# Performance work log

Measured on AMD Instinct MI355X. Metric: run time of the kernel, lower is better.

The kernel has to match this reference:

```python
import jax, jax.numpy as jnp
import numpy as np

B, T, N, E, H, L, K = 2, 32, 256, 1024, 16, 2, 256
MAXLEN = 512  # RelativeMultiheadAttention max_seq_len default
SCALES = (1, 2, 4)
TAU = 1.0


def setup_inputs() -> dict:
    key = jax.random.key(0)
    ks = jax.random.split(key, 9)
    s = 0.02
    A = 2 * L  # [layer0-spatial, layer0-temporal, layer1-spatial, layer1-temporal]
    return {
        "x": jax.random.normal(ks[0], (B, T, N, E), jnp.float32),
        "attn_wq": jax.random.normal(ks[1], (A, E, E), jnp.float32) * s,
        "attn_bq": jnp.zeros((A, E), jnp.float32),
        "attn_wk": jax.random.normal(ks[2], (A, E, E), jnp.float32) * s,
        "attn_bk": jnp.zeros((A, E), jnp.float32),
        "attn_wv": jax.random.normal(ks[3], (A, E, E), jnp.float32) * s,
        "attn_bv": jnp.zeros((A, E), jnp.float32),
        "attn_wd": jax.random.normal(ks[4], (A, E, E), jnp.float32) * s,
        "attn_bd": jnp.zeros((A, E), jnp.float32),
        "rel_bias": jax.random.normal(ks[5], (A, 2 * MAXLEN - 1, H), jnp.float32) * s,
        "sel_w": jax.random.normal(ks[6], (E, K), jnp.float32) * s,
        "sel_b": jnp.zeros((K,), jnp.float32),
    }


def _rel_attn(x, wq, bq, wk, bk, wv, bv, wd, bd, rb):
    # x: [Bx, S, E]; rb: [2*MAXLEN-1, H]
    Bx, S, _ = x.shape
    D = E // H
    q = (x @ wq + bq).reshape(Bx, S, H, D)
    k = (x @ wk + bk).reshape(Bx, S, H, D)
    v = (x @ wv + bv).reshape(Bx, S, H, D)
    scores = jnp.einsum('bshd,bthd->bhst', q, k) / jnp.sqrt(jnp.asarray(D, x.dtype))
    pos = jnp.arange(S)
    idx = pos[None, :] - pos[:, None] + (MAXLEN - 1)  # [S, S]
    bias = rb[idx]  # [S, S, H] gathered relative-position bias
    scores = scores + bias.transpose(2, 0, 1)[None]
    w = jax.nn.softmax(scores, axis=-1)
    ctx = jnp.einsum('bhst,bthd->bshd', w, v).reshape(Bx, S, E)
    return ctx @ wd + bd


def reference(x, attn_wq, attn_bq, attn_wk, attn_bk, attn_wv, attn_bv,
              attn_wd, attn_bd, rel_bias, sel_w, sel_b):
    h = x
    for l in range(L):
        # spatial attention over tokens within each frame
        i = 2 * l
        hs = h.reshape(B * T, N, E)
        hs = _rel_attn(hs, attn_wq[i], attn_bq[i], attn_wk[i], attn_bk[i],
                       attn_wv[i], attn_bv[i], attn_wd[i], attn_bd[i], rel_bias[i])
        # temporal attention across frames per spatial location
        j = 2 * l + 1
        ht = hs.reshape(B, T, N, E).transpose(0, 2, 1, 3).reshape(B * N, T, E)
        ht = _rel_attn(ht, attn_wq[j], attn_bq[j], attn_wk[j], attn_bk[j],
                       attn_wv[j], attn_bv[j], attn_wd[j], attn_bd[j], rel_bias[j])
        h = ht.reshape(B, N, T, E).transpose(0, 2, 1, 3)
    # DifferentiableTokenSelection: softmax-weighted pooling into K tokens
    flat = h.reshape(B, T * N, E)
    sc = flat @ sel_w + sel_b  # [B, T*N, K]
    wts = jax.nn.softmax(sc / TAU, axis=1)
    sel = jnp.einsum('bmk,bme->bke', wts, flat)  # [B, K, E]
    # multi-scale average pooling (kernel==stride==scale), concat along tokens
    outs = [sel.reshape(B, K // s, s, E).mean(axis=2) for s in SCALES]
    return jnp.concatenate(outs, axis=1)  # [B, K + K//2 + K//4, E]
```

## Files before the change

### kernel.cpp

```cpp
#include <hip/hip_runtime.h>
#include <stdint.h>


using f16x8 = __attribute__((ext_vector_type(8))) _Float16;
using f16x4 = __attribute__((ext_vector_type(4))) _Float16;
using f32x4 = __attribute__((ext_vector_type(4))) float;

__device__ __forceinline__ int tmap_dev(int m) {
    int bx = m >> 5;
    int s  = m & 31;
    int b  = bx >> 8;
    int n  = bx & 255;
    return (((b << 5) + s) << 8) + n;
}

__device__ __forceinline__ void load16(const _Float16* g, _Float16* l)
{
    __builtin_amdgcn_global_load_lds(
        (const __attribute__((address_space(1))) unsigned int*)g,
        (__attribute__((address_space(3))) unsigned int*)l,
        16, 0, 0);
}

__device__ __forceinline__ void split_f16(float v, _Float16& h, _Float16& l)
{
    h = (_Float16)v;
    l = (_Float16)(v - (float)h);
}

__global__ __launch_bounds__(256)
void conv_act(const float* __restrict__ src, _Float16* __restrict__ dh,
              _Float16* __restrict__ dl, int m_off)
{
    int idx = blockIdx.x * 256 + threadIdx.x;
    int e = idx << 3;
    int ml = e >> 10, col = e & 1023;
    const float* s = src + (size_t)(m_off + ml) * 1024 + col;
    float4 a = *(const float4*)s;
    float4 b = *(const float4*)(s + 4);
    float vv[8] = {a.x, a.y, a.z, a.w, b.x, b.y, b.z, b.w};
    f16x8 vh, vl;
    #pragma unroll
    for (int r = 0; r < 8; r++) {
        _Float16 h, l;
        split_f16(vv[r], h, l);
        vh[r] = h; vl[r] = l;
    }
    *(f16x8*)(dh + (size_t)ml * 1024 + col) = vh;
    *(f16x8*)(dl + (size_t)ml * 1024 + col) = vl;
}

__global__ __launch_bounds__(256)
void conv_wT(const float* __restrict__ W, _Float16* __restrict__ Th,
             _Float16* __restrict__ Tl, int ncols)
{
    __shared__ float Ls[64][65];
    const int n0 = blockIdx.x * 64, k0 = blockIdx.y * 64;
    const int t = threadIdx.x;
    const int kk = t >> 4, nn = (t & 15) << 2;
    #pragma unroll
    for (int i = 0; i < 4; i++) {
        float4 v = *(const float4*)(W + (size_t)(k0 + kk + 16 * i) * ncols + n0 + nn);
        Ls[kk + 16 * i][nn + 0] = v.x; Ls[kk + 16 * i][nn + 1] = v.y;
        Ls[kk + 16 * i][nn + 2] = v.z; Ls[kk + 16 * i][nn + 3] = v.w;
    }
    __syncthreads();
    const int nl = t >> 4, kc = (t & 15) << 2;
    #pragma unroll
    for (int i = 0; i < 4; i++) {
        int n = nl + 16 * i;
        f16x4 hh, ll;
        #pragma unroll
        for (int c = 0; c < 4; c++) {
            _Float16 h, l;
            split_f16(Ls[kc + c][n], h, l);
            hh[c] = h; ll[c] = l;
        }
        *(f16x4*)(Th + (size_t)(n0 + n) * 1024 + k0 + kc) = hh;
        *(f16x4*)(Tl + (size_t)(n0 + n) * 1024 + k0 + kc) = ll;
    }
}

template<int EPI>
__device__ __forceinline__ void gemm_core(
    const _Float16* __restrict__ Ah, const _Float16* __restrict__ Al,
    const _Float16* __restrict__ Wh, const _Float16* __restrict__ Wl,
    const float* __restrict__ bias,
    float* __restrict__ C, _Float16* __restrict__ Ch, _Float16* __restrict__ Cl,
    int ldc, int map_in, int m_off_in, int map_out, int m_off_out,
    int n0, int m0)
{
    __shared__ uint32_t smem_u[8512];
    _Float16* smem = (_Float16*)smem_u;
    _Float16* sAh = smem;
    _Float16* sAl = smem + 4096;
    _Float16* sBh = smem + 8192;
    _Float16* sBl = smem + 12288;

    const int tid = threadIdx.x;
    const int lane = tid & 63;
    const int wv = tid >> 6;
    const int fm = (wv >> 1) << 6;
    const int fn = (wv & 1) << 6;
    const int lm = lane & 15, lq = lane >> 4;

    f32x4 acc[4][4] = {};

    const int srow = tid >> 2;
    const int skc  = (tid & 3) << 3;
    const int gm0 = m_off_in + m0 + srow;
    const int gm1 = gm0 + 64;
    const int r0 = map_in ? tmap_dev(gm0) : gm0;
    const int r1 = map_in ? tmap_dev(gm1) : gm1;
    const _Float16* gAh0 = Ah + (size_t)r0 * 1024 + skc;
    const _Float16* gAh1 = Ah + (size_t)r1 * 1024 + skc;
    const _Float16* gAl0 = Al + (size_t)r0 * 1024 + skc;
    const _Float16* gAl1 = Al + (size_t)r1 * 1024 + skc;
    const _Float16* gB0 = Wh + (size_t)(n0 + srow) * 1024 + skc;
    const _Float16* gB1 = Wl + (size_t)(n0 + srow) * 1024 + skc;
    const int lo = tid << 3;

    for (int k0 = 0; k0 < 1024; k0 += 32) {
        load16(gAh0 + k0, sAh + lo);
        load16(gAh1 + k0, sAh + lo + 2048);
        load16(gAl0 + k0, sAl + lo);
        load16(gAl1 + k0, sAl + lo + 2048);
        load16(gB0 + k0,         sBh + lo);
        load16(gB0 + k0 + 65536, sBh + lo + 2048);
        load16(gB1 + k0,         sBl + lo);
        load16(gB1 + k0 + 65536, sBl + lo + 2048);
        __syncthreads();

        f16x8 ah[4], al[4], bh[4], bl[4];
        #pragma unroll
        for (int i = 0; i < 4; i++) {
            int ra = (fm + i * 16 + lm) * 32 + lq * 8;
            ah[i] = *(const f16x8*)(sAh + ra);
            al[i] = *(const f16x8*)(sAl + ra);
            int rb_ = (fn + i * 16 + lm) * 32 + lq * 8;
            bh[i] = *(const f16x8*)(sBh + rb_);
            bl[i] = *(const f16x8*)(sBl + rb_);
        }
        #pragma unroll
        for (int i = 0; i < 4; i++)
            #pragma unroll
            for (int j = 0; j < 4; j++) {
                acc[i][j] = __builtin_amdgcn_mfma_f32_16x16x32_f16(ah[i], bh[j], acc[i][j], 0, 0, 0);
                acc[i][j] = __builtin_amdgcn_mfma_f32_16x16x32_f16(ah[i], bl[j], acc[i][j], 0, 0, 0);
                acc[i][j] = __builtin_amdgcn_mfma_f32_16x16x32_f16(al[i], bh[j], acc[i][j], 0, 0, 0);
            }
        __syncthreads();
    }

    if (EPI == 0) {
        #pragma unroll
        for (int j = 0; j < 4; j++) {
            int n = n0 + fn + j * 16 + lm;
            float bb = bias[n];
            #pragma unroll
            for (int i = 0; i < 4; i++) {
                #pragma unroll
                for (int r = 0; r < 4; r++) {
                    int gm = m_off_out + m0 + fm + i * 16 + lq * 4 + r;
                    int row = map_out ? tmap_dev(gm) : gm;
                    C[(size_t)row * ldc + n] = acc[i][j][r] + bb;
                }
            }
        }
    }
}

__global__ __launch_bounds__(256, 2)
void gemm_f16s_f32(const _Float16* __restrict__ Ah, const _Float16* __restrict__ Al,
                   int map_in, int m_off_in,
                   const _Float16* __restrict__ Wh, const _Float16* __restrict__ Wl,
                   const float* __restrict__ bias, float* __restrict__ C, int ldc,
                   int map_out, int m_off_out)
{
    gemm_core<0>(Ah, Al, Wh, Wl, bias, C, nullptr, nullptr, ldc,
                 map_in, m_off_in, map_out, m_off_out,
                 blockIdx.x * 128, blockIdx.y * 128);
}

template<int EPI>
__device__ __forceinline__ void gemm256_core(
    uint32_t* __restrict__ smem_u,
    const _Float16* __restrict__ Ah, const _Float16* __restrict__ Al,
    const _Float16* __restrict__ Wh, const _Float16* __restrict__ Wl,
    const float* __restrict__ bias,
    _Float16* __restrict__ Ch, _Float16* __restrict__ Cl,
    int map_in, int m_off_in, int map_out, int m_off_out,
    int n0, int m0)
{
    _Float16* S = (_Float16*)smem_u;
    const int tid  = threadIdx.x;
    const int lane = tid & 63;
    const int wv = tid >> 6;
    const int wm = wv >> 1;
    const int fm = wm << 6;
    const int fn = (wv & 1) << 6;
    const int lm = lane & 15, lq = lane >> 4;
    const int ko = ((lq ^ ((lm >> 1) & 3)) << 3);

    f32x4 acc[4][4] = {};

    const int srow = tid >> 2;
    const int scol = (((tid & 3) ^ ((tid >> 3) & 3)) << 3);
    const int gm0 = m_off_in + m0 + srow;
    const int gm1 = gm0 + 128;
    const int r0 = map_in ? tmap_dev(gm0) : gm0;
    const int r1 = map_in ? tmap_dev(gm1) : gm1;
    const _Float16* gAh0 = Ah + (size_t)r0 * 1024 + scol;
    const _Float16* gAh1 = Ah + (size_t)r1 * 1024 + scol;
    const _Float16* gAl0 = Al + (size_t)r0 * 1024 + scol;
    const _Float16* gAl1 = Al + (size_t)r1 * 1024 + scol;
    const _Float16* gBh  = Wh + (size_t)(n0 + srow) * 1024 + scol;
    const _Float16* gBl  = Wl + (size_t)(n0 + srow) * 1024 + scol;
    const int lo = tid << 3;

    auto stage_part = [&](int t, int b, int part) {
        const int k0 = t << 5;
        _Float16* d = S + b * 24576;
        if (part == 0) {
            load16(gAh0 + k0, d + lo);
            load16(gAh1 + k0, d + 4096  + lo);
        } else if (part == 1) {
            load16(gAl0 + k0, d + 8192  + lo);
            load16(gAl1 + k0, d + 12288 + lo);
        } else {
            load16(gBh  + k0, d + 16384 + lo);
            load16(gBl  + k0, d + 20480 + lo);
        }
    };

    auto kstep = [&](int t, int cb, int sb, int vmN) {
        const _Float16* c = S + cb * 24576;
        f16x8 ah[4], al[4];

        #pragma unroll
        for (int i = 0; i < 4; i++) {
            int ra = (fm + i * 16 + lm) * 32 + ko;
            ah[i] = *(const f16x8*)(c + ra);
            al[i] = *(const f16x8*)(c + 8192 + ra);
        }
        {
            int rb = (fn + lm) * 32 + ko;
            f16x8 bh = *(const f16x8*)(c + 16384 + rb);
            f16x8 bl = *(const f16x8*)(c + 20480 + rb);
            if (sb >= 0) stage_part(t + 2, sb, 0);
            __builtin_amdgcn_s_barrier();
            asm volatile("s_waitcnt lgkmcnt(0)" ::: "memory");
            __builtin_amdgcn_sched_barrier(0);
            __builtin_amdgcn_s_setprio(1);
            #pragma unroll
            for (int i = 0; i < 4; i++) {
                acc[i][0] = __builtin_amdgcn_mfma_f32_16x16x32_f16(ah[i], bh, acc[i][0], 0, 0, 0);
                acc[i][0] = __builtin_amdgcn_mfma_f32_16x16x32_f16(ah[i], bl, acc[i][0], 0, 0, 0);
                acc[i][0] = __builtin_amdgcn_mfma_f32_16x16x32_f16(al[i], bh, acc[i][0], 0, 0, 0);
            }
            __builtin_amdgcn_s_setprio(0);
            __builtin_amdgcn_s_barrier();
        }

        #pragma unroll
        for (int j = 1; j < 4; j++) {
            int rb = (fn + j * 16 + lm) * 32 + ko;
            f16x8 bh = *(const f16x8*)(c + 16384 + rb);
            f16x8 bl = *(const f16x8*)(c + 20480 + rb);
            if (j < 3) {
                if (sb >= 0) stage_part(t + 2, sb, j);
            } else {
                if (vmN == 6)      asm volatile("s_waitcnt vmcnt(6)" ::: "memory");
                else if (vmN == 0) asm volatile("s_waitcnt vmcnt(0)" ::: "memory");
            }
            __builtin_amdgcn_s_barrier();
            asm volatile("s_waitcnt lgkmcnt(0)" ::: "memory");
            __builtin_amdgcn_sched_barrier(0);
            __builtin_amdgcn_s_setprio(1);
            #pragma unroll
            for (int i = 0; i < 4; i++) {
                acc[i][j] = __builtin_amdgcn_mfma_f32_16x16x32_f16(ah[i], bh, acc[i][j], 0, 0, 0);
                acc[i][j] = __builtin_amdgcn_mfma_f32_16x16x32_f16(ah[i], bl, acc[i][j], 0, 0, 0);
                acc[i][j] = __builtin_amdgcn_mfma_f32_16x16x32_f16(al[i], bh, acc[i][j], 0, 0, 0);
            }
            __builtin_amdgcn_s_setprio(0);
            __builtin_amdgcn_s_barrier();
        }
    };

    #pragma unroll
    for (int p = 0; p < 3; p++) stage_part(0, 0, p);
    #pragma unroll
    for (int p = 0; p < 3; p++) stage_part(1, 1, p);
    asm volatile("s_waitcnt vmcnt(6)" ::: "memory");
    __builtin_amdgcn_s_barrier();

    #pragma unroll 1
    for (int tt = 0; tt < 30; tt += 3) {
        kstep(tt + 0, 0, 2, 6);
        kstep(tt + 1, 1, 0, 6);
        kstep(tt + 2, 2, 1, 6);
    }
    kstep(30, 0, -1, 0);
    kstep(31, 1, -1, -1);

    if (EPI == 1) {
        #pragma unroll 1
        for (int q = 0; q < 4; q++) {
            __syncthreads();
            if (wm == q) {
                #pragma unroll
                for (int j = 0; j < 4; j++) {
                    int ncol = fn + j * 16 + lm;
                    float bb = bias[n0 + ncol];
                    #pragma unroll
                    for (int i = 0; i < 4; i++) {
                        #pragma unroll
                        for (int r = 0; r < 4; r++) {
                            float v = acc[i][j][r] + bb;
                            _Float16 h, l;
                            split_f16(v, h, l);
                            uint32_t ph = (uint32_t)__builtin_bit_cast(unsigned short, h);
                            uint32_t pl = (uint32_t)__builtin_bit_cast(unsigned short, l);
                            smem_u[(i * 16 + lq * 4 + r) * 132 + ncol] = ph | (pl << 16);
                        }
                    }
                }
            }
            __syncthreads();
            #pragma unroll
            for (int g = 0; g < 2; g++) {
                int u = tid + g * 512;
                int rl = u >> 4;
                int c8 = (u & 15) << 3;
                uint32_t p[8];
                #pragma unroll
                for (int x = 0; x < 8; x++) p[x] = smem_u[rl * 132 + c8 + x];
                f16x8 hh, ll;
                #pragma unroll
                for (int x = 0; x < 8; x++) {
                    hh[x] = __builtin_bit_cast(_Float16, (unsigned short)(p[x] & 0xffff));
                    ll[x] = __builtin_bit_cast(_Float16, (unsigned short)(p[x] >> 16));
                }
                int gm = m_off_out + m0 + q * 64 + rl;
                int row = map_out ? tmap_dev(gm) : gm;
                *(f16x8*)(Ch + (size_t)row * 1024 + n0 + c8) = hh;
                *(f16x8*)(Cl + (size_t)row * 1024 + n0 + c8) = ll;
            }
        }
    } else {
        #pragma unroll 1
        for (int q = 0; q < 4; q++) {
            __syncthreads();
            if (wm == q) {
                #pragma unroll
                for (int j = 0; j < 4; j++) {
                    int ncol = fn + j * 16 + lm;
                    float bb = bias[n0 + ncol];
                    #pragma unroll
                    for (int i = 0; i < 4; i++) {
                        #pragma unroll
                        for (int r = 0; r < 4; r++) {
                            float v = acc[i][j][r] + bb;
                            _Float16 h, l;
                            split_f16(v, h, l);
                            uint32_t ph = (uint32_t)__builtin_bit_cast(unsigned short, h);
                            uint32_t pl = (uint32_t)__builtin_bit_cast(unsigned short, l);
                            smem_u[(i * 16 + lq * 4 + r) * 129 + ncol] = ph | (pl << 16);
                        }
                    }
                }
            }
            __syncthreads();
            #pragma unroll
            for (int g = 0; g < 4; g++) {
                int u = tid + g * 512;
                int nn = u >> 4;
                int mg = (u & 15) << 2;
                uint32_t p0 = smem_u[(mg + 0) * 129 + nn];
                uint32_t p1 = smem_u[(mg + 1) * 129 + nn];
                uint32_t p2 = smem_u[(mg + 2) * 129 + nn];
                uint32_t p3 = smem_u[(mg + 3) * 129 + nn];
                f16x4 hh, ll;
                hh[0] = __builtin_bit_cast(_Float16, (unsigned short)(p0 & 0xffff));
                hh[1] = __builtin_bit_cast(_Float16, (unsigned short)(p1 & 0xffff));
                hh[2] = __builtin_bit_cast(_Float16, (unsigned short)(p2 & 0xffff));
                hh[3] = __builtin_bit_cast(_Float16, (unsigned short)(p3 & 0xffff));
                ll[0] = __builtin_bit_cast(_Float16, (unsigned short)(p0 >> 16));
                ll[1] = __builtin_bit_cast(_Float16, (unsigned short)(p1 >> 16));
                ll[2] = __builtin_bit_cast(_Float16, (unsigned short)(p2 >> 16));
                ll[3] = __builtin_bit_cast(_Float16, (unsigned short)(p3 >> 16));
                size_t off = (size_t)(n0 + nn) * 8192 + (m0 + q * 64 + mg);
                *(f16x4*)(Ch + off) = hh;
                *(f16x4*)(Cl + off) = ll;
            }
        }
    }
}

__global__ __launch_bounds__(512, 2)
void gemm_qkv256(const _Float16* __restrict__ Ah, const _Float16* __restrict__ Al,
                 int map_in, int m_off_in,
                 const _Float16* __restrict__ WTh, const _Float16* __restrict__ WTl,
                 const float* __restrict__ bq, const float* __restrict__ bk,
                 const float* __restrict__ bv,
                 _Float16* __restrict__ Qh, _Float16* __restrict__ Ql,
                 _Float16* __restrict__ Kh, _Float16* __restrict__ Kl,
                 _Float16* __restrict__ VTh, _Float16* __restrict__ VTl)
{
    __shared__ uint32_t smem_u[36864];
    const int bid = blockIdx.x;
    const int wg = (bid & 7) * 96 + (bid >> 3);
    const int z = wg >> 8;
    const int rem = wg & 255;
    const int m0 = (rem >> 3) << 8;
    const int n0 = (rem & 7) << 7;
    const _Float16* wh = WTh + (size_t)z * 1048576;
    const _Float16* wl = WTl + (size_t)z * 1048576;
    if (z < 2) {
        const float* bb = (z == 0) ? bq : bk;
        _Float16* oh = (z == 0) ? Qh : Kh;
        _Float16* ol = (z == 0) ? Ql : Kl;
        gemm256_core<1>(smem_u, Ah, Al, wh, wl, bb, oh, ol,
                        map_in, m_off_in, 0, 0, n0, m0);
    } else {
        gemm256_core<3>(smem_u, Ah, Al, wh, wl, bv, VTh, VTl,
                        map_in, m_off_in, 0, 0, n0, m0);
    }
}

__global__ __launch_bounds__(512, 2)
void gemm_h256(const _Float16* __restrict__ Ah, const _Float16* __restrict__ Al,
               int map_in, int m_off_in,
               const _Float16* __restrict__ Wh, const _Float16* __restrict__ Wl,
               const float* __restrict__ bias,
               _Float16* __restrict__ Ch, _Float16* __restrict__ Cl,
               int map_out, int m_off_out)
{
    __shared__ uint32_t smem_u[36864];
    const int bid = blockIdx.x;
    const int wg = (bid & 7) * 32 + (bid >> 3);
    const int m0 = (wg >> 3) << 8;
    const int n0 = (wg & 7) << 7;
    gemm256_core<1>(smem_u, Ah, Al, Wh, Wl, bias, Ch, Cl,
                    map_in, m_off_in, map_out, m_off_out, n0, m0);
}

__global__ __launch_bounds__(256, 2)
void attn_s_m(const _Float16* __restrict__ Qh, const _Float16* __restrict__ Ql,
              const _Float16* __restrict__ Kh, const _Float16* __restrict__ Kl,
              const _Float16* __restrict__ VTh, const _Float16* __restrict__ VTl,
              const float* __restrict__ RB,
              _Float16* __restrict__ Ch, _Float16* __restrict__ Cl)
{
    __shared__ _Float16 sKh[2048], sKl[2048];
    __shared__ _Float16 sVh[2560], sVl[2560];
    __shared__ _Float16 sPh[4][2560], sPl[4][2560];
    __shared__ float Bt[512];

    const int tid = threadIdx.x;
    const int lane = tid & 63;
    const int w = tid >> 6;
    const int lm = lane & 15, lq = lane >> 4;
    const int frame = blockIdx.x;
    const int h = blockIdx.y;
    const int rowbase = frame * 256;

    #pragma unroll
    for (int l = 0; l < 2; l++) {
        int idx = tid + l * 256;
        if (idx < 511) Bt[idx] = RB[(size_t)(256 + idx) * 16 + h];
    }

    f16x8 qbh[4][2], qbl[4][2];
    #pragma unroll
    for (int st = 0; st < 4; st++)
        #pragma unroll
        for (int kk = 0; kk < 2; kk++) {
            size_t qo = (size_t)(rowbase + w * 64 + st * 16 + lm) * 1024
                        + h * 64 + kk * 32 + lq * 8;
            qbh[st][kk] = *(const f16x8*)(Qh + qo);
            qbl[st][kk] = *(const f16x8*)(Ql + qo);
        }

    f32x4 cacc[4][4] = {};
    float lsum[4] = {0.f, 0.f, 0.f, 0.f};
    _Float16* Ph = sPh[w];
    _Float16* Pl = sPl[w];

    const int skrow = tid >> 3, skd = (tid & 7) << 3;
    const int svrow = tid >> 2, svj = (tid & 3) << 3;

    for (int jc = 0; jc < 8; jc++) {
        __syncthreads();
        {
            size_t ko = (size_t)(rowbase + jc * 32 + skrow) * 1024 + h * 64 + skd;
            *(f16x8*)(sKh + skrow * 64 + skd) = *(const f16x8*)(Kh + ko);
            *(f16x8*)(sKl + skrow * 64 + skd) = *(const f16x8*)(Kl + ko);
            size_t vo = (size_t)(h * 64 + svrow) * 8192 + rowbase + jc * 32 + svj;
            *(f16x8*)(sVh + svrow * 40 + svj) = *(const f16x8*)(VTh + vo);
            *(f16x8*)(sVl + svrow * 40 + svj) = *(const f16x8*)(VTl + vo);
        }
        __syncthreads();

        f32x4 sacc[2][4] = {};
        #pragma unroll
        for (int jt = 0; jt < 2; jt++) {
            f16x8 kah[2], kal[2];
            #pragma unroll
            for (int kk = 0; kk < 2; kk++) {
                int ra = (jt * 16 + lm) * 64 + kk * 32 + lq * 8;
                kah[kk] = *(const f16x8*)(sKh + ra);
                kal[kk] = *(const f16x8*)(sKl + ra);
            }
            #pragma unroll
            for (int st = 0; st < 4; st++)
                #pragma unroll
                for (int kk = 0; kk < 2; kk++) {
                    sacc[jt][st] = __builtin_amdgcn_mfma_f32_16x16x32_f16(kah[kk], qbh[st][kk], sacc[jt][st], 0, 0, 0);
                    sacc[jt][st] = __builtin_amdgcn_mfma_f32_16x16x32_f16(kah[kk], qbl[st][kk], sacc[jt][st], 0, 0, 0);
                    sacc[jt][st] = __builtin_amdgcn_mfma_f32_16x16x32_f16(kal[kk], qbh[st][kk], sacc[jt][st], 0, 0, 0);
                }
        }

        #pragma unroll
        for (int jt = 0; jt < 2; jt++)
            #pragma unroll
            for (int st = 0; st < 4; st++) {
                f16x4 p4h, p4l;
                #pragma unroll
                for (int r = 0; r < 4; r++) {
                    int j = jc * 32 + jt * 16 + lq * 4 + r;
                    int s = w * 64 + st * 16 + lm;
                    float p = __expf(sacc[jt][st][r] * 0.125f + Bt[j - s + 255]);
                    lsum[st] += p;
                    _Float16 hp, lp;
                    split_f16(p, hp, lp);
                    p4h[r] = hp; p4l[r] = lp;
                }
                int pa = (st * 16 + lm) * 40 + jt * 16 + lq * 4;
                *(f16x4*)(Ph + pa) = p4h;
                *(f16x4*)(Pl + pa) = p4l;
            }

        #pragma unroll
        for (int st = 0; st < 4; st++) {
            int pb = (st * 16 + lm) * 40 + lq * 8;
            f16x8 pbh = *(const f16x8*)(Ph + pb);
            f16x8 pbl = *(const f16x8*)(Pl + pb);
            #pragma unroll
            for (int dt = 0; dt < 4; dt++) {
                int va = (dt * 16 + lm) * 40 + lq * 8;
                f16x8 vah = *(const f16x8*)(sVh + va);
                f16x8 val = *(const f16x8*)(sVl + va);
                cacc[dt][st] = __builtin_amdgcn_mfma_f32_16x16x32_f16(vah, pbh, cacc[dt][st], 0, 0, 0);
                cacc[dt][st] = __builtin_amdgcn_mfma_f32_16x16x32_f16(vah, pbl, cacc[dt][st], 0, 0, 0);
                cacc[dt][st] = __builtin_amdgcn_mfma_f32_16x16x32_f16(val, pbh, cacc[dt][st], 0, 0, 0);
            }
        }
    }

    float inv[4];
    #pragma unroll
    for (int st = 0; st < 4; st++) {
        float t = lsum[st];
        t += __shfl_xor(t, 16);
        t += __shfl_xor(t, 32);
        inv[st] = 1.0f / t;
    }

    #pragma unroll
    for (int st = 0; st < 4; st++)
        #pragma unroll
        for (int dt = 0; dt < 4; dt++) {
            f16x4 oh, ol;
            #pragma unroll
            for (int r = 0; r < 4; r++) {
                _Float16 hp, lp;
                split_f16(cacc[dt][st][r] * inv[st], hp, lp);
                oh[r] = hp; ol[r] = lp;
            }
            size_t oo = (size_t)(rowbase + w * 64 + st * 16 + lm) * 1024
                        + h * 64 + dt * 16 + lq * 4;
            *(f16x4*)(Ch + oo) = oh;
            *(f16x4*)(Cl + oo) = ol;
        }
}

__global__ __launch_bounds__(256, 2)
void attn_t_m(const _Float16* __restrict__ Qh, const _Float16* __restrict__ Ql,
              const _Float16* __restrict__ Kh, const _Float16* __restrict__ Kl,
              const _Float16* __restrict__ VTh, const _Float16* __restrict__ VTl,
              const float* __restrict__ RB,
              _Float16* __restrict__ Ch, _Float16* __restrict__ Cl)
{
    __shared__ _Float16 sPh[4][1280], sPl[4][1280];
    __shared__ float Bt[64];

    const int tid = threadIdx.x;
    const int lane = tid & 63;
    const int w = tid >> 6;
    const int lm = lane & 15, lq = lane >> 4;
    const int h = blockIdx.y;
    const int bx = blockIdx.x * 4 + w;
    const int rowbase = bx * 32;

    if (tid < 63) Bt[tid] = RB[(size_t)(480 + tid) * 16 + h];
    __syncthreads();

    f16x8 qbh[2][2], qbl[2][2];
    #pragma unroll
    for (int st = 0; st < 2; st++)
        #pragma unroll
        for (int kk = 0; kk < 2; kk++) {
            size_t qo = (size_t)(rowbase + st * 16 + lm) * 1024 + h * 64 + kk * 32 + lq * 8;
            qbh[st][kk] = *(const f16x8*)(Qh + qo);
            qbl[st][kk] = *(const f16x8*)(Ql + qo);
        }

    f32x4 sacc[2][2] = {};
    #pragma unroll
    for (int jt = 0; jt < 2; jt++) {
        f16x8 kah[2], kal[2];
        #pragma unroll
        for (int kk = 0; kk < 2; kk++) {
            size_t ko = (size_t)(rowbase + jt * 16 + lm) * 1024 + h * 64 + kk * 32 + lq * 8;
            kah[kk] = *(const f16x8*)(Kh + ko);
            kal[kk] = *(const f16x8*)(Kl + ko);
        }
        #pragma unroll
        for (int st = 0; st < 2; st++)
            #pragma unroll
            for (int kk = 0; kk < 2; kk++) {
                sacc[jt][st] = __builtin_amdgcn_mfma_f32_16x16x32_f16(kah[kk], qbh[st][kk], sacc[jt][st], 0, 0, 0);
                sacc[jt][st] = __builtin_amdgcn_mfma_f32_16x16x32_f16(kah[kk], qbl[st][kk], sacc[jt][st], 0, 0, 0);
                sacc[jt][st] = __builtin_amdgcn_mfma_f32_16x16x32_f16(kal[kk], qbh[st][kk], sacc[jt][st], 0, 0, 0);
            }
    }

    float lsum[2] = {0.f, 0.f};
    _Float16* Ph = sPh[w];
    _Float16* Pl = sPl[w];
    #pragma unroll
    for (int jt = 0; jt < 2; jt++)
        #pragma unroll
        for (int st = 0; st < 2; st++) {
            f16x4 p4h, p4l;
            #pragma unroll
            for (int r = 0; r < 4; r++) {
                int j = jt * 16 + lq * 4 + r;
                int s = st * 16 + lm;
                float p = __expf(sacc[jt][st][r] * 0.125f + Bt[j - s + 31]);
                lsum[st] += p;
                _Float16 hp, lp;
                split_f16(p, hp, lp);
                p4h[r] = hp; p4l[r] = lp;
            }
            int pa = (st * 16 + lm) * 40 + jt * 16 + lq * 4;
            *(f16x4*)(Ph + pa) = p4h;
            *(f16x4*)(Pl + pa) = p4l;
        }

    f16x8 vah[4], val[4];
    #pragma unroll
    for (int dt = 0; dt < 4; dt++) {
        size_t vo = (size_t)(h * 64 + dt * 16 + lm) * 8192 + rowbase + lq * 8;
        vah[dt] = *(const f16x8*)(VTh + vo);
        val[dt] = *(const f16x8*)(VTl + vo);
    }
    f32x4 cacc[4][2] = {};
    #pragma unroll
    for (int st = 0; st < 2; st++) {
        int pb = (st * 16 + lm) * 40 + lq * 8;
        f16x8 pbh = *(const f16x8*)(Ph + pb);
        f16x8 pbl = *(const f16x8*)(Pl + pb);
        #pragma unroll
        for (int dt = 0; dt < 4; dt++) {
            cacc[dt][st] = __builtin_amdgcn_mfma_f32_16x16x32_f16(vah[dt], pbh, cacc[dt][st], 0, 0, 0);
            cacc[dt][st] = __builtin_amdgcn_mfma_f32_16x16x32_f16(vah[dt], pbl, cacc[dt][st], 0, 0, 0);
            cacc[dt][st] = __builtin_amdgcn_mfma_f32_16x16x32_f16(val[dt], pbh, cacc[dt][st], 0, 0, 0);
        }
    }

    float inv[2];
    #pragma unroll
    for (int st = 0; st < 2; st++) {
        float t = lsum[st];
        t += __shfl_xor(t, 16);
        t += __shfl_xor(t, 32);
        inv[st] = 1.0f / t;
    }

    #pragma unroll
    for (int st = 0; st < 2; st++)
        #pragma unroll
        for (int dt = 0; dt < 4; dt++) {
            f16x4 oh, ol;
            #pragma unroll
            for (int r = 0; r < 4; r++) {
                _Float16 hp, lp;
                split_f16(cacc[dt][st][r] * inv[st], hp, lp);
                oh[r] = hp; ol[r] = lp;
            }
            size_t oo = (size_t)(rowbase + st * 16 + lm) * 1024 + h * 64 + dt * 16 + lq * 4;
            *(f16x4*)(Ch + oo) = oh;
            *(f16x4*)(Cl + oo) = ol;
        }
}

__global__ __launch_bounds__(256)
void colsum_part_kernel(const float* __restrict__ SC, float* __restrict__ P)
{
    int bid = blockIdx.x;
    int b = bid >> 7, chunk = bid & 127;
    int base = b * 8192 + chunk * 64;
    int k = threadIdx.x;
    float sum = 0.0f;
    for (int r = 0; r < 64; r++)
        sum += __expf(SC[(size_t)(base + r) * 256 + k]);
    P[(size_t)bid * 256 + k] = sum;
}

__global__ __launch_bounds__(256)
void colsum_reduce_kernel(const float* __restrict__ P, float* __restrict__ CS)
{
    int b = blockIdx.x;
    int k = threadIdx.x;
    float s = 0.0f;
    for (int c = 0; c < 128; c++)
        s += P[(size_t)(b * 128 + c) * 256 + k];
    CS[b * 256 + k] = s;
}

__global__ __launch_bounds__(256)
void trans_wts(const float* __restrict__ SC, const float* __restrict__ CS,
               _Float16* __restrict__ Th, _Float16* __restrict__ Tl)
{
    __shared__ float L[64][65];
    const int mt = blockIdx.x * 64;
    const int kt = blockIdx.y * 64;
    const int b  = mt >> 13;
    const int ml = mt & 8191;
    const int tid = threadIdx.x;
    #pragma unroll
    for (int l = 0; l < 4; l++) {
        int idx = tid + 256 * l;
        int r = idx >> 4, c4 = (idx & 15) << 2;
        float4 v = *(const float4*)(SC + (size_t)(mt + r) * 256 + kt + c4);
        L[r][c4 + 0] = __expf(v.x); L[r][c4 + 1] = __expf(v.y);
        L[r][c4 + 2] = __expf(v.z); L[r][c4 + 3] = __expf(v.w);
    }
    __syncthreads();
    #pragma unroll
    for (int l = 0; l < 4; l++) {
        int idx = tid + 256 * l;
        int rk = idx >> 4, c4 = (idx & 15) << 2;
        float inv = 1.0f / CS[b * 256 + kt + rk];
        f16x4 hh, ll;
        #pragma unroll
        for (int u = 0; u < 4; u++) {
            _Float16 h, l2;
            split_f16(L[c4 + u][rk] * inv, h, l2);
            hh[u] = h; ll[u] = l2;
        }
        size_t o = ((size_t)b * 256 + kt + rk) * 8192 + ml + c4;
        *(f16x4*)(Th + o) = hh;
        *(f16x4*)(Tl + o) = ll;
    }
}

__global__ __launch_bounds__(256)
void trans_f16(const _Float16* __restrict__ Sh, const _Float16* __restrict__ Sl,
               _Float16* __restrict__ Th, _Float16* __restrict__ Tl)
{
    __shared__ _Float16 L[64][72];
    const int mt = blockIdx.x * 64, et = blockIdx.y * 64;
    const _Float16* S = blockIdx.z ? Sl : Sh;
    _Float16* T = blockIdx.z ? Tl : Th;
    const int tid = threadIdx.x;
    #pragma unroll
    for (int l = 0; l < 2; l++) {
        int v = tid * 2 + l;
        int r = v >> 3, c8 = (v & 7) << 3;
        *(f16x8*)&L[r][c8] = *(const f16x8*)(S + (size_t)(mt + r) * 1024 + et + c8);
    }
    __syncthreads();
    #pragma unroll
    for (int l = 0; l < 2; l++) {
        int v = tid * 2 + l;
        int r = v >> 3, c8 = (v & 7) << 3;
        f16x8 o;
        #pragma unroll
        for (int u = 0; u < 8; u++) o[u] = L[c8 + u][r];
        *(f16x8*)(T + (size_t)(et + r) * 16384 + mt + c8) = o;
    }
}

__global__ __launch_bounds__(256, 2)
void gemm_selm(const _Float16* __restrict__ Wth, const _Float16* __restrict__ Wtl,
               const _Float16* __restrict__ Hth, const _Float16* __restrict__ Htl,
               float* __restrict__ P)
{
    __shared__ _Float16 sAh[4096], sAl[4096], sBh[4096], sBl[4096];
    const int tid = threadIdx.x;
    const int lane = tid & 63;
    const int wv = tid >> 6;
    const int fm = (wv >> 1) << 6;
    const int fn = (wv & 1) << 6;
    const int lm = lane & 15, lq = lane >> 4;
    const int n0 = blockIdx.x * 128;
    const int m0 = blockIdx.y * 128;
    const int z  = blockIdx.z;
    const int b = z >> 3, sp = z & 7;

    f32x4 acc[4][4] = {};

    const int srow = tid >> 2;
    const int skc  = (tid & 3) << 3;
    const _Float16* gAh0 = Wth + ((size_t)b * 256 + m0 + srow) * 8192 + sp * 1024 + skc;
    const _Float16* gAl0 = Wtl + ((size_t)b * 256 + m0 + srow) * 8192 + sp * 1024 + skc;
    const _Float16* gB0 = Hth + (size_t)(n0 + srow) * 16384 + b * 8192 + sp * 1024 + skc;
    const _Float16* gB1 = Htl + (size_t)(n0 + srow) * 16384 + b * 8192 + sp * 1024 + skc;
    const int lo = tid << 3;

    for (int k0 = 0; k0 < 1024; k0 += 32) {
        load16(gAh0 + k0,          sAh + lo);
        load16(gAh0 + k0 + 524288, sAh + lo + 2048);
        load16(gAl0 + k0,          sAl + lo);
        load16(gAl0 + k0 + 524288, sAl + lo + 2048);
        load16(gB0 + k0,           sBh + lo);
        load16(gB0 + k0 + 1048576, sBh + lo + 2048);
        load16(gB1 + k0,           sBl + lo);
        load16(gB1 + k0 + 1048576, sBl + lo + 2048);
        __syncthreads();

        f16x8 ah[4], al[4], bh[4], bl[4];
        #pragma unroll
        for (int i = 0; i < 4; i++) {
            int ra = (fm + i * 16 + lm) * 32 + lq * 8;
            ah[i] = *(const f16x8*)(sAh + ra);
            al[i] = *(const f16x8*)(sAl + ra);
            int rb_ = (fn + i * 16 + lm) * 32 + lq * 8;
            bh[i] = *(const f16x8*)(sBh + rb_);
            bl[i] = *(const f16x8*)(sBl + rb_);
        }
        #pragma unroll
        for (int i = 0; i < 4; i++)
            #pragma unroll
            for (int j = 0; j < 4; j++) {
                acc[i][j] = __builtin_amdgcn_mfma_f32_16x16x32_f16(ah[i], bh[j], acc[i][j], 0, 0, 0);
                acc[i][j] = __builtin_amdgcn_mfma_f32_16x16x32_f16(ah[i], bl[j], acc[i][j], 0, 0, 0);
                acc[i][j] = __builtin_amdgcn_mfma_f32_16x16x32_f16(al[i], bh[j], acc[i][j], 0, 0, 0);
            }
        __syncthreads();
    }

    float* Pz = P + (size_t)z * 262144;
    #pragma unroll
    for (int j = 0; j < 4; j++) {
        int n = n0 + fn + j * 16 + lm;
        #pragma unroll
        for (int i = 0; i < 4; i++)
            #pragma unroll
            for (int r = 0; r < 4; r++) {
                int k = m0 + fm + i * 16 + lq * 4 + r;
                Pz[(size_t)k * 1024 + n] = acc[i][j][r];
            }
    }
}

__global__ __launch_bounds__(256)
void sel_reduce(const float* __restrict__ P, float* __restrict__ SEL)
{
    int idx4 = blockIdx.x * 256 + threadIdx.x;
    int e = idx4 << 2;
    int b = e >> 18;
    int rest = e & 262143;
    const float* p = P + (size_t)(b * 8) * 262144 + rest;
    float4 acc = {0.f, 0.f, 0.f, 0.f};
    #pragma unroll
    for (int s = 0; s < 8; s++) {
        float4 v = *(const float4*)(p + (size_t)s * 262144);
        acc.x += v.x; acc.y += v.y; acc.z += v.z; acc.w += v.w;
    }
    *(float4*)(SEL + e) = acc;
}

__global__ __launch_bounds__(256)
void pool_kernel(const float* __restrict__ SEL, float* __restrict__ out)
{
    int i4 = blockIdx.x * 256 + threadIdx.x;
    int e  = i4 << 2;
    int row = e >> 10;
    int b = row / 448;
    int r = row - b * 448;
    int c = e & 1023;
    const float* sb = SEL + (size_t)b * (256 * 1024);
    float4 o;
    if (r < 256) {
        o = *(const float4*)(sb + (size_t)r * 1024 + c);
    } else if (r < 384) {
        int r2 = (r - 256) * 2;
        float4 x0 = *(const float4*)(sb + (size_t)r2 * 1024 + c);
        float4 x1 = *(const float4*)(sb + (size_t)(r2 + 1) * 1024 + c);
        o.x = 0.5f * (x0.x + x1.x); o.y = 0.5f * (x0.y + x1.y);
        o.z = 0.5f * (x0.z + x1.z); o.w = 0.5f * (x0.w + x1.w);
    } else {
        int r4 = (r - 384) * 4;
        float4 x0 = *(const float4*)(sb + (size_t)(r4 + 0) * 1024 + c);
        float4 x1 = *(const float4*)(sb + (size_t)(r4 + 1) * 1024 + c);
        float4 x2 = *(const float4*)(sb + (size_t)(r4 + 2) * 1024 + c);
        float4 x3 = *(const float4*)(sb + (size_t)(r4 + 3) * 1024 + c);
        o.x = 0.25f * (x0.x + x1.x + x2.x + x3.x);
        o.y = 0.25f * (x0.y + x1.y + x2.y + x3.y);
        o.z = 0.25f * (x0.z + x1.z + x2.z + x3.z);
        o.w = 0.25f * (x0.w + x1.w + x2.w + x3.w);
    }
    *(float4*)(out + e) = o;
}

extern "C" void kernel_launch(void* const* d_in, const int* in_sizes, int n_in,
                              void* d_out, int out_size, void* d_ws, size_t ws_size,
                              hipStream_t stream)
{
    const float* x    = (const float*)d_in[0];
    const float* wq   = (const float*)d_in[1];
    const float* bq   = (const float*)d_in[2];
    const float* wk   = (const float*)d_in[3];
    const float* bk   = (const float*)d_in[4];
    const float* wv   = (const float*)d_in[5];
    const float* bv   = (const float*)d_in[6];
    const float* wd   = (const float*)d_in[7];
    const float* bd   = (const float*)d_in[8];
    const float* rb   = (const float*)d_in[9];
    const float* selw = (const float*)d_in[10];
    const float* selb = (const float*)d_in[11];
    float* out = (float*)d_out;

    float* base = (float*)d_ws;
    _Float16* Hh  = (_Float16*)base;
    _Float16* Hl  = Hh + 16777216;
    _Float16* Qh  = (_Float16*)(base + 16777216);
    _Float16* Ql  = Qh + 8388608;
    _Float16* Kh  = Ql + 8388608;
    _Float16* Kl  = Kh + 8388608;
    _Float16* VTh = (_Float16*)(base + 33554432);
    _Float16* VTl = VTh + 8388608;
    _Float16* CXh = (_Float16*)(base + 41943040);
    _Float16* CXl = CXh + 8388608;
    _Float16* WTh = (_Float16*)(base + 50331648);
    _Float16* WTl = WTh + 4194304;
    _Float16* Ah  = (_Float16*)(base + 54525952);
    _Float16* Al  = Ah + 8388608;
    float* SC   = (float*)Qh;
    float* Pp   = (float*)Kh;
    float* SEL  = (float*)Kl;
    float* PART = SEL + 524288;
    float* CSUM = PART + 65536;
    _Float16* WTTh = CXh;
    _Float16* WTTl = CXl;
    _Float16* HTh  = Ah;
    _Float16* HTl  = VTh;

    const dim3 blk(256);
    const dim3 blk2(512);

    for (int a = 0; a < 4; a++) {
        const int mi = (a & 1);
        const size_t wo = (size_t)a * 1048576;
        const int bo = a * 1024;
        const float* rba = rb + (size_t)a * 1023 * 16;

        conv_wT<<<dim3(16, 16), blk, 0, stream>>>(wq + wo, WTh,           WTl,           1024);
        conv_wT<<<dim3(16, 16), blk, 0, stream>>>(wk + wo, WTh + 1048576, WTl + 1048576, 1024);
        conv_wT<<<dim3(16, 16), blk, 0, stream>>>(wv + wo, WTh + 2097152, WTl + 2097152, 1024);
        conv_wT<<<dim3(16, 16), blk, 0, stream>>>(wd + wo, WTh + 3145728, WTl + 3145728, 1024);

        for (int c = 0; c < 2; c++) {
            const int mo = c * 8192;
            const _Float16 *sH, *sL;
            int sm, so;
            if (a == 0) {
                conv_act<<<4096, blk, 0, stream>>>(x, Ah, Al, mo);
                sH = Ah; sL = Al; sm = 0; so = 0;
            } else {
                sH = Hh; sL = Hl; sm = mi; so = mo;
            }
            gemm_qkv256<<<dim3(768), blk2, 0, stream>>>(
                sH, sL, sm, so, WTh, WTl, bq + bo, bk + bo, bv + bo,
                Qh, Ql, Kh, Kl, VTh, VTl);
            if (mi == 0)
                attn_s_m<<<dim3(32, 16), blk, 0, stream>>>(Qh, Ql, Kh, Kl, VTh, VTl, rba, CXh, CXl);
            else
                attn_t_m<<<dim3(64, 16), blk, 0, stream>>>(Qh, Ql, Kh, Kl, VTh, VTl, rba, CXh, CXl);
            gemm_h256<<<dim3(256), blk2, 0, stream>>>(
                CXh, CXl, 0, 0, WTh + 3145728, WTl + 3145728, bd + bo, Hh, Hl, mi, mo);
        }
    }

    conv_wT<<<dim3(4, 16), blk, 0, stream>>>(selw, WTh, WTl, 256);
    gemm_f16s_f32<<<dim3(2, 128), blk, 0, stream>>>(
        Hh, Hl, 0, 0, WTh, WTl, selb, SC, 256, 0, 0);
    colsum_part_kernel<<<256, blk, 0, stream>>>(SC, PART);
    colsum_reduce_kernel<<<2, blk, 0, stream>>>(PART, CSUM);
    trans_wts<<<dim3(256, 4), blk, 0, stream>>>(SC, CSUM, WTTh, WTTl);
    trans_f16<<<dim3(256, 16, 2), blk, 0, stream>>>(Hh, Hl, HTh, HTl);
    gemm_selm<<<dim3(8, 2, 16), blk, 0, stream>>>(WTTh, WTTl, HTh, HTl, Pp);
    sel_reduce<<<512, blk, 0, stream>>>(Pp, SEL);
    pool_kernel<<<896, blk, 0, stream>>>(SEL, out);
}
```

Before: 2.184 ms.

## Double-buffer GEMM fragments in registers and use one barrier per k-step

Restructures the split-f16 GEMM main loop. Each k-step now prefetches the next tile's LDS fragments into a second register set and issues all global-to-LDS loads for tile t+2 up front. It then runs all 48 MFMAs, followed by a single vmcnt(0) wait and one barrier, replacing the previous four barrier pairs per k-step. The goal is fewer barriers and overlap of LDS reads with MFMA work. The cost is twice the fragment registers, which may lower occupancy, and a full vmcnt(0) wait every step.

```diff
diff --git a/kernel.cpp b/kernel.cpp
--- a/kernel.cpp
+++ b/kernel.cpp
@@ -218,91 +218,74 @@
     const _Float16* gBl  = Wl + (size_t)(n0 + srow) * 1024 + scol;
     const int lo = tid << 3;
 
-    auto stage_part = [&](int t, int b, int part) {
+    auto stage = [&](int t, int b) {
         const int k0 = t << 5;
         _Float16* d = S + b * 24576;
-        if (part == 0) {
-            load16(gAh0 + k0, d + lo);
-            load16(gAh1 + k0, d + 4096  + lo);
-        } else if (part == 1) {
-            load16(gAl0 + k0, d + 8192  + lo);
-            load16(gAl1 + k0, d + 12288 + lo);
-        } else {
-            load16(gBh  + k0, d + 16384 + lo);
-            load16(gBl  + k0, d + 20480 + lo);
-        }
+        load16(gAh0 + k0, d + lo);
+        load16(gAh1 + k0, d + 4096  + lo);
+        load16(gAl0 + k0, d + 8192  + lo);
+        load16(gAl1 + k0, d + 12288 + lo);
+        load16(gBh  + k0, d + 16384 + lo);
+        load16(gBl  + k0, d + 20480 + lo);
     };
 
-    auto kstep = [&](int t, int cb, int sb, int vmN) {
-        const _Float16* c = S + cb * 24576;
-        f16x8 ah[4], al[4];
-
+    auto ldfrags = [&](const _Float16* c,
+                       f16x8 (&xah)[4], f16x8 (&xal)[4],
+                       f16x8 (&xbh)[4], f16x8 (&xbl)[4]) {
         #pragma unroll
         for (int i = 0; i < 4; i++) {
             int ra = (fm + i * 16 + lm) * 32 + ko;
-            ah[i] = *(const f16x8*)(c + ra);
-            al[i] = *(const f16x8*)(c + 8192 + ra);
-        }
-        {
-            int rb = (fn + lm) * 32 + ko;
-            f16x8 bh = *(const f16x8*)(c + 16384 + rb);
-            f16x8 bl = *(const f16x8*)(c + 20480 + rb);
-            if (sb >= 0) stage_part(t + 2, sb, 0);
-            __builtin_amdgcn_s_barrier();
-            asm volatile("s_waitcnt lgkmcnt(0)" ::: "memory");
-            __builtin_amdgcn_sched_barrier(0);
-            __builtin_amdgcn_s_setprio(1);
-            #pragma unroll
-            for (int i = 0; i < 4; i++) {
-                acc[i][0] = __builtin_amdgcn_mfma_f32_16x16x32_f16(ah[i], bh, acc[i][0], 0, 0, 0);
-                acc[i][0] = __builtin_amdgcn_mfma_f32_16x16x32_f16(ah[i], bl, acc[i][0], 0, 0, 0);
-                acc[i][0] = __builtin_amdgcn_mfma_f32_16x16x32_f16(al[i], bh, acc[i][0], 0, 0, 0);
-            }
-            __builtin_amdgcn_s_setprio(0);
-            __builtin_amdgcn_s_barrier();
-        }
-
-        #pragma unroll
-        for (int j = 1; j < 4; j++) {
-            int rb = (fn + j * 16 + lm) * 32 + ko;
-            f16x8 bh = *(const f16x8*)(c + 16384 + rb);
-            f16x8 bl = *(const f16x8*)(c + 20480 + rb);
-            if (j < 3) {
-                if (sb >= 0) stage_part(t + 2, sb, j);
-            } else {
-                if (vmN == 6)      asm volatile("s_waitcnt vmcnt(6)" ::: "memory");
-                else if (vmN == 0) asm volatile("s_waitcnt vmcnt(0)" ::: "memory");
-            }
-            __builtin_amdgcn_s_barrier();
-            asm volatile("s_waitcnt lgkmcnt(0)" ::: "memory");
-            __builtin_amdgcn_sched_barrier(0);
-            __builtin_amdgcn_s_setprio(1);
-            #pragma unroll
-            for (int i = 0; i < 4; i++) {
-                acc[i][j] = __builtin_amdgcn_mfma_f32_16x16x32_f16(ah[i], bh, acc[i][j], 0, 0, 0);
-                acc[i][j] = __builtin_amdgcn_mfma_f32_16x16x32_f16(ah[i], bl, acc[i][j], 0, 0, 0);
-                acc[i][j] = __builtin_amdgcn_mfma_f32_16x16x32_f16(al[i], bh, acc[i][j], 0, 0, 0);
-            }
-            __builtin_amdgcn_s_setprio(0);
-            __builtin_amdgcn_s_barrier();
+            xah[i] = *(const f16x8*)(c + ra);
+            xal[i] = *(const f16x8*)(c + 8192 + ra);
+            int rb = (fn + i * 16 + lm) * 32 + ko;
+            xbh[i] = *(const f16x8*)(c + 16384 + rb);
+            xbl[i] = *(const f16x8*)(c + 20480 + rb);
         }
     };
 
-    #pragma unroll
-    for (int p = 0; p < 3; p++) stage_part(0, 0, p);
-    #pragma unroll
-    for (int p = 0; p < 3; p++) stage_part(1, 1, p);
-    asm volatile("s_waitcnt vmcnt(6)" ::: "memory");
+    f16x8 ahA[4], alA[4], bhA[4], blA[4];
+    f16x8 ahB[4], alB[4], bhB[4], blB[4];
+
+    auto kstep = [&](int t, int nxtbuf, int stagebuf,
+                     f16x8 (&cah)[4], f16x8 (&cal)[4],
+                     f16x8 (&cbh)[4], f16x8 (&cbl)[4],
+                     f16x8 (&nah)[4], f16x8 (&nal)[4],
+                     f16x8 (&nbh)[4], f16x8 (&nbl)[4],
+                     bool prefetch, bool dostage) {
+        if (prefetch) ldfrags(S + nxtbuf * 24576, nah, nal, nbh, nbl);
+        if (dostage) stage(t + 2, stagebuf);
+        __builtin_amdgcn_sched_barrier(0);
+        __builtin_amdgcn_s_setprio(1);
+        #pragma unroll
+        for (int i = 0; i < 4; i++)
+            #pragma unroll
+            for (int j = 0; j < 4; j++) {
+                acc[i][j] = __builtin_amdgcn_mfma_f32_16x16x32_f16(cah[i], cbh[j], acc[i][j], 0, 0, 0);
+                acc[i][j] = __builtin_amdgcn_mfma_f32_16x16x32_f16(cah[i], cbl[j], acc[i][j], 0, 0, 0);
+                acc[i][j] = __builtin_amdgcn_mfma_f32_16x16x32_f16(cal[i], cbh[j], acc[i][j], 0, 0, 0);
+            }
+        __builtin_amdgcn_s_setprio(0);
+        asm volatile("s_waitcnt vmcnt(0)" ::: "memory");
+        __builtin_amdgcn_s_barrier();
+    };
+
+    stage(0, 0);
+    stage(1, 1);
+    asm volatile("s_waitcnt vmcnt(0)" ::: "memory");
     __builtin_amdgcn_s_barrier();
+    ldfrags(S, ahA, alA, bhA, blA);
 
     #pragma unroll 1
-    for (int tt = 0; tt < 30; tt += 3) {
-        kstep(tt + 0, 0, 2, 6);
-        kstep(tt + 1, 1, 0, 6);
-        kstep(tt + 2, 2, 1, 6);
-    }
-    kstep(30, 0, -1, 0);
-    kstep(31, 1, -1, -1);
+    for (int tt = 0; tt < 30; tt += 6) {
+        kstep(tt + 0, 1, 2, ahA, alA, bhA, blA, ahB, alB, bhB, blB, true, true);
+        kstep(tt + 1, 2, 0, ahB, alB, bhB, blB, ahA, alA, bhA, blA, true, true);
+        kstep(tt + 2, 0, 1, ahA, alA, bhA, blA, ahB, alB, bhB, blB, true, true);
+        kstep(tt + 3, 1, 2, ahB, alB, bhB, blB, ahA, alA, bhA, blA, true, true);
+        kstep(tt + 4, 2, 0, ahA, alA, bhA, blA, ahB, alB, bhB, blB, true, true);
+        kstep(tt + 5, 0, 1, ahB, alB, bhB, blB, ahA, alA, bhA, blA, true, true);
+    }
+    kstep(30, 1, 0, ahA, alA, bhA, blA, ahB, alB, bhB, blB, true,  false);
+    kstep(31, 0, 0, ahB, alB, bhB, blB, ahA, alA, bhA, blA, false, false);
 
     if (EPI == 1) {
         #pragma unroll 1
```

Result: slower. 2.515 ms (+15.1%).
